# Kernel optimization log

Measured on AMD Instinct MI355X. Metric: run time of the kernel, lower is better.

Reference implementation:

```python
import jax, jax.numpy as jnp
import numpy as np

M1 = 12; M2 = 12; WIDTH = 32; NR = 16; GROUPS = 2; EPS = 1e-5
AND_M = 5; AND_LAM = 1e-4; AND_MAXIT = 16; AND_BETA = 1.0
B = 4; H = 192; W = 192


def group_norm(x, w, b, groups=GROUPS, eps=EPS):
    bb, c, hh, ww = x.shape
    xg = x.reshape(bb, groups, c // groups, hh, ww)
    mu = xg.mean(axis=(2, 3, 4), keepdims=True)
    var = xg.var(axis=(2, 3, 4), keepdims=True)
    xn = ((xg - mu) / jnp.sqrt(var + eps)).reshape(bb, c, hh, ww)
    return xn * w[None, :, None, None] + b[None, :, None, None]


def spectral_conv(z, w1, w2):
    bb, c, hh, ww = z.shape
    zf = jnp.fft.rfft2(z, axes=(-2, -1))  # (B,C,H,W//2+1) complex64
    top = jnp.einsum('bixy,ioxy->boxy', zf[:, :, :M1, :M2], w1)
    bot = jnp.einsum('bixy,ioxy->boxy', zf[:, :, hh - M1:, :M2], w2)
    out = jnp.zeros(zf.shape, zf.dtype)
    out = out.at[:, :, :M1, :M2].set(top).at[:, :, hh - M1:, :M2].set(bot)
    return jnp.fft.irfft2(out, s=(hh, ww), axes=(-2, -1))


def f_block(z, xin, p):
    (conv_w, gnw, gnb, q_w, q_b, w1r, w1i, w2r, w2i,
     w0w, w0b, n1w, n1b, n2w, n2b) = p
    # ConvInjection: conv3x3 -> GroupNorm -> channel Linear -> sigmoid
    xi = jax.lax.conv_general_dilated(xin, conv_w, (1, 1), 'SAME',
                                      dimension_numbers=('NCHW', 'OIHW', 'NCHW'))
    xi = group_norm(xi, gnw, gnb)
    xi = jax.nn.sigmoid(jnp.einsum('bnhw,dn->bdhw', xi, q_w) + q_b[None, :, None, None])
    # FourierLayer: spectral conv + 1x1 conv, gelu
    y1 = spectral_conv(z, jax.lax.complex(w1r, w1i), jax.lax.complex(w2r, w2i))
    y2 = jnp.einsum('bchw,oc->bohw', z, w0w) + w0b[None, :, None, None]
    y = jax.nn.gelu(y1 + y2, approximate=False)
    return group_norm(jax.nn.relu(z + group_norm(xi + y, n1w, n1b)), n2w, n2b)


def anderson(f, x0, m=AND_M, lam=AND_LAM, max_iter=AND_MAXIT, beta=AND_BETA):
    """Anderson acceleration; fixed iteration count (tol early-exit omitted)."""
    shp = x0.shape
    bsz = shp[0]
    fv = lambda v: f(v.reshape(shp)).reshape(bsz, -1)
    x0v = x0.reshape(bsz, -1)
    d = x0v.shape[1]
    f0 = fv(x0v)
    f1 = fv(f0)
    X = jnp.zeros((bsz, m, d), x0.dtype).at[:, 0].set(x0v).at[:, 1].set(f0)
    Fm = jnp.zeros((bsz, m, d), x0.dtype).at[:, 0].set(f0).at[:, 1].set(f1)
    last = 1
    for k in range(2, max_iter):
        n = min(k, m)
        G = Fm[:, :n] - X[:, :n]
        Hk = jnp.zeros((bsz, n + 1, n + 1), x0.dtype)
        Hk = Hk.at[:, 0, 1:].set(1.0).at[:, 1:, 0].set(1.0)
        Hk = Hk.at[:, 1:, 1:].set(jnp.einsum('bnd,bmd->bnm', G, G)
                                  + lam * jnp.eye(n, dtype=x0.dtype)[None])
        yk = jnp.zeros((bsz, n + 1, 1), x0.dtype).at[:, 0, 0].set(1.0)
        alpha = jnp.linalg.solve(Hk, yk)[:, 1:, 0]  # (B, n)
        xnew = (beta * jnp.einsum('bn,bnd->bd', alpha, Fm[:, :n])
                + (1.0 - beta) * jnp.einsum('bn,bnd->bd', alpha, X[:, :n]))
        X = X.at[:, k % m].set(xnew)
        Fm = Fm.at[:, k % m].set(fv(xnew))
        last = k % m
    return X[:, last].reshape(shp)


def setup_inputs():
    key = jax.random.key(0)
    ks = jax.random.split(key, 16)
    scale = 1.0 / (WIDTH * WIDTH)
    u = lambda k, shp, s: jax.random.uniform(k, shp, jnp.float32, -s, s)
    return {
        'x': jax.random.normal(ks[0], (B, 1, H, W), jnp.float32),
        'fc0_w': u(ks[1], (WIDTH, 1), 1.0),
        'fc0_b': u(ks[2], (WIDTH,), 1.0),
        'conv_w': 0.01 * jax.random.normal(ks[3], (NR, WIDTH, 3, 3), jnp.float32),
        'inj_gn_w': jnp.ones((NR,), jnp.float32),
        'inj_gn_b': jnp.zeros((NR,), jnp.float32),
        'q_w': 0.01 * jax.random.normal(ks[4], (WIDTH, NR), jnp.float32),
        'q_b': u(ks[5], (WIDTH,), 0.25),
        'sw1r': scale * jax.random.uniform(ks[6], (WIDTH, WIDTH, M1, M2), jnp.float32),
        'sw1i': scale * jax.random.uniform(ks[7], (WIDTH, WIDTH, M1, M2), jnp.float32),
        'sw2r': scale * jax.random.uniform(ks[8], (WIDTH, WIDTH, M1, M2), jnp.float32),
        'sw2i': scale * jax.random.uniform(ks[9], (WIDTH, WIDTH, M1, M2), jnp.float32),
        'w0_w': u(ks[10], (WIDTH, WIDTH), 1.0 / np.sqrt(WIDTH)),
        'w0_b': u(ks[11], (WIDTH,), 1.0 / np.sqrt(WIDTH)),
        'n1_w': jnp.ones((WIDTH,), jnp.float32),
        'n1_b': jnp.zeros((WIDTH,), jnp.float32),
        'n2_w': jnp.ones((WIDTH,), jnp.float32),
        'n2_b': jnp.zeros((WIDTH,), jnp.float32),
        'bn_w': jnp.ones((WIDTH,), jnp.float32),
        'bn_b': jnp.zeros((WIDTH,), jnp.float32),
        'fc1_w': u(ks[12], (32, WIDTH), 1.0 / np.sqrt(WIDTH)),
        'fc1_b': u(ks[13], (32,), 1.0 / np.sqrt(WIDTH)),
        'fc2_w': u(ks[14], (1, 32), 1.0 / np.sqrt(32.0)),
        'fc2_b': u(ks[15], (1,), 1.0 / np.sqrt(32.0)),
    }


def reference(x, fc0_w, fc0_b, conv_w, inj_gn_w, inj_gn_b, q_w, q_b,
              sw1r, sw1i, sw2r, sw2i, w0_w, w0_b, n1_w, n1_b, n2_w, n2_b,
              bn_w, bn_b, fc1_w, fc1_b, fc2_w, fc2_b):
    xin = jnp.einsum('bchw,oc->bohw', x, fc0_w) + fc0_b[None, :, None, None]
    p = (conv_w, inj_gn_w, inj_gn_b, q_w, q_b, sw1r, sw1i, sw2r, sw2i,
         w0_w, w0_b, n1_w, n1_b, n2_w, n2_b)
    z_star = anderson(lambda z: f_block(z, xin, p), jnp.zeros_like(xin))
    z = f_block(z_star, xin, p)
    # BatchNorm2d (training-mode batch statistics, biased var)
    mu = z.mean(axis=(0, 2, 3), keepdims=True)
    var = z.var(axis=(0, 2, 3), keepdims=True)
    zb = (z - mu) / jnp.sqrt(var + EPS) * bn_w[None, :, None, None] + bn_b[None, :, None, None]
    h1 = jax.nn.gelu(jnp.einsum('bchw,oc->bohw', zb, fc1_w) + fc1_b[None, :, None, None],
                     approximate=False)
    return jnp.einsum('bchw,oc->bohw', h1, fc2_w) + fc2_b[None, :, None, None]
```

## Files before the change

### kernel.cpp

```cpp
#include <hip/hip_runtime.h>
#include <math.h>

#ifndef M_PI
#define M_PI 3.14159265358979323846
#endif

#define BBc 4
#define CCc 32
#define NRk 16
#define HHc 192
#define WWc 192
#define HWc 36864
#define DDi 1179648
#define M1c 12
#define EPSc 1e-5f

static const size_t DDs = (size_t)DDi;

#define SZ_T   ((size_t)4718592)
#define SZ_ZC  ((size_t)589824)
#define SZ_ZF  ((size_t)73728)
#define SZ_WT  ((size_t)589824)
#define SZ_TAB ((size_t)4992)

#define OFF_XC   ((size_t)0)
#define OFF_XI   (OFF_XC + SZ_T)
#define OFF_F    (OFF_XI + SZ_T)
#define OFF_G    (OFF_F + 5 * SZ_T)
#define OFF_ZC   (OFF_G + 5 * SZ_T)
#define OFF_ZF   (OFF_ZC + SZ_ZC)
#define OFF_MO   (OFF_ZF + SZ_ZF)
#define OFF_TM   (OFF_MO + SZ_ZF)
#define OFF_WT   (OFF_TM + SZ_ZC)
#define OFF_TAB  (OFF_WT + SZ_WT)
#define OFF_STAT (OFF_TAB + SZ_TAB)
#define A_XI0  OFF_G

#define NSLICE  32
#define NGSLICE 16
#define ST_EV   1024
#define ST_INJ   (16 * ST_EV)
#define ST_BN    (ST_INJ + 16)
#define ST_GRAM  (ST_BN + 64)
#define ST_ALPHA (ST_GRAM + NGSLICE * 60)
#define ST_TOTAL (ST_ALPHA + 20)

__device__ __forceinline__ float bf2f(unsigned short u) {
    return __uint_as_float(((unsigned int)u) << 16);
}
__device__ __forceinline__ unsigned short f2bf(float f) {
    unsigned int u = __float_as_uint(f);
    unsigned int r = (u + 0x7FFFu + ((u >> 16) & 1u)) >> 16;
    return (unsigned short)r;
}

__global__ void k_zero(float* p, int n) {
    int i = blockIdx.x * blockDim.x + threadIdx.x;
    if (i < n) p[i] = 0.f;
}

__global__ void k_tables(float* tab) {
    int i = blockIdx.x * blockDim.x + threadIdx.x;
    if (i < 13 * 192) {
        int k = i / 192, x = i % 192;
        double th = 2.0 * M_PI * (double)(k * x) / 192.0;
        tab[i] = (float)cos(th);
        tab[13 * 192 + i] = (float)sin(th);
    }
}

__global__ void k_wt(const float* __restrict__ w1r, const float* __restrict__ w1i,
                     const float* __restrict__ w2r, const float* __restrict__ w2i,
                     float* __restrict__ wt) {
    int idx = blockIdx.x * 256 + threadIdx.x;
    if (idx >= 24 * 12 * 1024) return;
    int o = idx & 31;
    int i = (idx >> 5) & 31;
    int ky = (idx >> 10) % 12;
    int j = idx / (12 * 1024);
    const float* wr;
    const float* wi;
    int x;
    if (j < 12) { wr = w1r; wi = w1i; x = j; }
    else        { wr = w2r; wi = w2i; x = j - 12; }
    int src = ((i * 32 + o) * 12 + x) * 12 + ky;
    size_t dst = (((size_t)ky * 24 + j) * 1024 + i * 32 + o) * 2;
    wt[dst] = wr[src];
    wt[dst + 1] = wi[src];
}

__global__ void k_ew(const float* __restrict__ cw, const float* __restrict__ fc0w,
                     const float* __restrict__ fc0b, float* __restrict__ ewb) {
    int i = threadIdx.x;
    if (i >= 144) return;
    int n = i / 9, t = i % 9;
    float ew = 0.f, eb = 0.f;
    for (int c = 0; c < 32; ++c) {
        float k = cw[(size_t)(n * CCc + c) * 9 + t];
        ew += k * fc0w[c];
        eb += k * fc0b[c];
    }
    ewb[i] = ew;
    ewb[144 + i] = eb;
}

__global__ __launch_bounds__(192) void k_conv2(const float* __restrict__ x,
                                               const float* __restrict__ ewb,
                                               float* __restrict__ xi0) {
    int b = blockIdx.x / HHc, h = blockIdx.x % HHc;
    __shared__ float sm[3 * 194];
    __shared__ float ews[144], ebs[144];
    int w = threadIdx.x;
    for (int i = threadIdx.x; i < 3 * 194; i += 192) {
        int r = i / 194, col = (i % 194) - 1;
        int hr = h + r - 1;
        float v = 0.f;
        if (hr >= 0 && hr < HHc && col >= 0 && col < WWc)
            v = x[(size_t)b * HWc + (size_t)hr * WWc + col];
        sm[i] = v;
    }
    if (threadIdx.x < 144) {
        ews[threadIdx.x] = ewb[threadIdx.x];
        ebs[threadIdx.x] = ewb[144 + threadIdx.x];
    }
    __syncthreads();
    float xv[9], mk[9];
#pragma unroll
    for (int r = 0; r < 3; ++r) {
        int hr = h + r - 1;
        bool rok = (hr >= 0 && hr < HHc);
#pragma unroll
        for (int dx = 0; dx < 3; ++dx) {
            int wx = w + dx - 1;
            bool ok = rok && (wx >= 0) && (wx < WWc);
            xv[r * 3 + dx] = sm[r * 194 + (w + dx)];
            mk[r * 3 + dx] = ok ? 1.f : 0.f;
        }
    }
#pragma unroll
    for (int n = 0; n < 16; ++n) {
        float acc = 0.f;
#pragma unroll
        for (int t = 0; t < 9; ++t)
            acc += ews[n * 9 + t] * xv[t] + mk[t] * ebs[n * 9 + t];
        xi0[((size_t)b * NRk + n) * HWc + (size_t)h * WWc + w] = acc;
    }
}

__global__ void k_binstats(const float* __restrict__ src, float* __restrict__ stats,
                           int binsize, int blocksPerBin) {
    int bin = blockIdx.x / blocksPerBin, sub = blockIdx.x % blocksPerBin;
    const float* p = src + (size_t)bin * binsize;
    float s = 0.f, q = 0.f;
    for (int i = sub * blockDim.x + threadIdx.x; i < binsize; i += blocksPerBin * blockDim.x) {
        float v = p[i];
        s += v;
        q += v * v;
    }
    for (int o = 32; o; o >>= 1) { s += __shfl_down(s, o); q += __shfl_down(q, o); }
    __shared__ float rs[4], rq[4];
    int wid = threadIdx.x >> 6, lane = threadIdx.x & 63;
    if (lane == 0) { rs[wid] = s; rq[wid] = q; }
    __syncthreads();
    if (threadIdx.x == 0) {
        int nw = blockDim.x >> 6;
        float ts = 0.f, tq = 0.f;
        for (int i = 0; i < nw; ++i) { ts += rs[i]; tq += rq[i]; }
        atomicAdd(&stats[bin * 2], ts);
        atomicAdd(&stats[bin * 2 + 1], tq);
    }
}

__global__ __launch_bounds__(192) void k_xi(const float* __restrict__ xi0,
                                            const float* __restrict__ stats,
                                            const float* __restrict__ gnw, const float* __restrict__ gnb,
                                            const float* __restrict__ qw, const float* __restrict__ qb,
                                            float* __restrict__ xi) {
    int b = blockIdx.x / HHc, h = blockIdx.x % HHc;
    int w = threadIdx.x;
    const float Ninv = 1.f / (8.f * HWc);
    float tn[16];
#pragma unroll
    for (int n = 0; n < 16; ++n) {
        int g = n >> 3;
        float su = stats[(b * 2 + g) * 2], sq = stats[(b * 2 + g) * 2 + 1];
        float mu = su * Ninv;
        float var = sq * Ninv - mu * mu;
        float inv = rsqrtf(var + EPSc);
        float v = xi0[((size_t)b * NRk + n) * HWc + (size_t)h * WWc + w];
        tn[n] = (v - mu) * inv * gnw[n] + gnb[n];
    }
#pragma unroll
    for (int d = 0; d < 32; ++d) {
        float acc = qb[d];
        const float* row = qw + d * 16;
#pragma unroll
        for (int n = 0; n < 16; ++n) acc += tn[n] * row[n];
        xi[((size_t)b * CCc + d) * HWc + (size_t)h * WWc + w] = 1.f / (1.f + expf(-acc));
    }
}


__global__ __launch_bounds__(192) void k_dftw(const float* __restrict__ z0,
                                              const float* __restrict__ tab,
                                              float* __restrict__ Zc) {
    int bc = blockIdx.x / 24;
    int hg = blockIdx.x % 24;
    int b = bc >> 5, c = bc & 31;
    const float* zp = z0 + (size_t)b * DDs + (size_t)c * HWc + (size_t)hg * 8 * WWc;
    __shared__ float rows[8 * 196];
    __shared__ float tb[24 * 196];
    const float4* zq = (const float4*)zp;
    for (int i4 = threadIdx.x; i4 < 384; i4 += 192) {
        float4 v = zq[i4];
        int r = i4 / 48, col = (i4 % 48) * 4;
        *(float4*)&rows[r * 196 + col] = v;
    }
    for (int i4 = threadIdx.x; i4 < 1152; i4 += 192) {
        int rr = i4 / 48, col = (i4 % 48) * 4;
        const float* src = (rr < 12) ? &tab[rr * 192 + col] : &tab[2496 + (rr - 12) * 192 + col];
        *(float4*)&tb[rr * 196 + col] = *(const float4*)src;
    }
    __syncthreads();
    int t = threadIdx.x;
    int r = t / 24, q = t % 24, ky = q >> 1, isim = q & 1;
    const float* tbp = tb + (isim ? (12 + ky) * 196 : ky * 196);
    const float* rowp = rows + r * 196;
    float a0 = 0.f, a1 = 0.f, a2 = 0.f, a3 = 0.f;
#pragma unroll
    for (int w2 = 0; w2 < WWc; w2 += 4) {
        a0 += rowp[w2] * tbp[w2];
        a1 += rowp[w2 + 1] * tbp[w2 + 1];
        a2 += rowp[w2 + 2] * tbp[w2 + 2];
        a3 += rowp[w2 + 3] * tbp[w2 + 3];
    }
    float acc = (a0 + a1) + (a2 + a3);
    if (isim) acc = -acc;
    int h = hg * 8 + r;
    Zc[(((size_t)ky * 128 + bc) * HHc + h) * 2 + isim] = acc;
}

__global__ __launch_bounds__(192) void k_dftwx(const float* __restrict__ F,
                                               const float* __restrict__ gram,
                                               const float* __restrict__ tab,
                                               float* __restrict__ xc,
                                               float* __restrict__ Zc,
                                               int n) {
    int bc = blockIdx.x / 24;
    int hg = blockIdx.x % 24;
    int b = bc >> 5, c = bc & 31;
    __shared__ float rows[8 * 196];
    __shared__ float tb[24 * 196];
    __shared__ float gs[15];
    __shared__ float alf[5];
    for (int i4 = threadIdx.x; i4 < 1152; i4 += 192) {
        int rr = i4 / 48, col = (i4 % 48) * 4;
        const float* src = (rr < 12) ? &tab[rr * 192 + col] : &tab[2496 + (rr - 12) * 192 + col];
        *(float4*)&tb[rr * 196 + col] = *(const float4*)src;
    }
    if (threadIdx.x < 15) {
        float v = 0.f;
        for (int s2 = 0; s2 < NGSLICE; ++s2) v += gram[s2 * 60 + b * 15 + threadIdx.x];
        gs[threadIdx.x] = v;
    }
    __syncthreads();
    if (threadIdx.x == 0) {
        float H[5][5];
#pragma unroll
        for (int i = 0; i < 5; ++i)
#pragma unroll
            for (int j = 0; j <= i; ++j) {
                float v;
                if (i < n && j < n) v = gs[i * (i + 1) / 2 + j] + ((i == j) ? 1e-4f : 0.f);
                else                v = (i == j) ? 1.f : 0.f;
                H[i][j] = v;
                H[j][i] = v;
            }
        float L[5][5], D[5], w[5], y[5];
#pragma unroll
        for (int j = 0; j < 5; ++j) {
            float d = H[j][j];
#pragma unroll
            for (int k2 = 0; k2 < j; ++k2) d -= L[j][k2] * L[j][k2] * D[k2];
            D[j] = d;
#pragma unroll
            for (int i = j + 1; i < 5; ++i) {
                float v = H[i][j];
#pragma unroll
                for (int k2 = 0; k2 < j; ++k2) v -= L[i][k2] * L[j][k2] * D[k2];
                L[i][j] = v / d;
            }
        }
#pragma unroll
        for (int i = 0; i < 5; ++i) {
            float v = (i < n) ? 1.f : 0.f;
#pragma unroll
            for (int k2 = 0; k2 < i; ++k2) v -= L[i][k2] * w[k2];
            w[i] = v;
        }
#pragma unroll
        for (int i = 4; i >= 0; --i) {
            float v = w[i] / D[i];
#pragma unroll
            for (int k2 = i + 1; k2 < 5; ++k2) v -= L[k2][i] * y[k2];
            y[i] = v;
        }
        float sum = y[0] + y[1] + y[2] + y[3] + y[4];
        float inv = 1.f / sum;
#pragma unroll
        for (int j = 0; j < 5; ++j) alf[j] = (j < n) ? y[j] * inv : 0.f;
    }
    __syncthreads();
    float a0 = alf[0], a1 = alf[1], a2 = alf[2], a3 = alf[3], a4 = alf[4];

    size_t elem = (size_t)b * DDs + (size_t)c * HWc + (size_t)hg * 8 * WWc;
    int off4 = (int)(elem >> 2);
    const int sq4 = 1179648;
    const float4* F4 = (const float4*)F;
    float4* xc4 = (float4*)xc;
    if (n == 5) {
        for (int i4 = threadIdx.x; i4 < 384; i4 += 192) {
            float4 f0 = F4[off4 + i4];
            float4 f1 = F4[sq4 + off4 + i4];
            float4 f2 = F4[2 * sq4 + off4 + i4];
            float4 f3 = F4[3 * sq4 + off4 + i4];
            float4 f4v = F4[4 * sq4 + off4 + i4];
            float4 v;
            v.x = a0 * f0.x + a1 * f1.x + a2 * f2.x + a3 * f3.x + a4 * f4v.x;
            v.y = a0 * f0.y + a1 * f1.y + a2 * f2.y + a3 * f3.y + a4 * f4v.y;
            v.z = a0 * f0.z + a1 * f1.z + a2 * f2.z + a3 * f3.z + a4 * f4v.z;
            v.w = a0 * f0.w + a1 * f1.w + a2 * f2.w + a3 * f3.w + a4 * f4v.w;
            xc4[off4 + i4] = v;
            int r = i4 / 48, col = (i4 % 48) * 4;
            *(float4*)&rows[r * 196 + col] = v;
        }
    } else {
        for (int i4 = threadIdx.x; i4 < 384; i4 += 192) {
            float4 f0 = F4[off4 + i4];
            float4 f1 = F4[sq4 + off4 + i4];
            float4 v;
            v.x = a0 * f0.x + a1 * f1.x;
            v.y = a0 * f0.y + a1 * f1.y;
            v.z = a0 * f0.z + a1 * f1.z;
            v.w = a0 * f0.w + a1 * f1.w;
            if (n >= 3) {
                float4 f2 = F4[2 * sq4 + off4 + i4];
                v.x += a2 * f2.x; v.y += a2 * f2.y; v.z += a2 * f2.z; v.w += a2 * f2.w;
            }
            if (n >= 4) {
                float4 f3 = F4[3 * sq4 + off4 + i4];
                v.x += a3 * f3.x; v.y += a3 * f3.y; v.z += a3 * f3.z; v.w += a3 * f3.w;
            }
            xc4[off4 + i4] = v;
            int r = i4 / 48, col = (i4 % 48) * 4;
            *(float4*)&rows[r * 196 + col] = v;
        }
    }
    __syncthreads();
    int t = threadIdx.x;
    int r = t / 24, q = t % 24, ky = q >> 1, isim = q & 1;
    const float* tbp = tb + (isim ? (12 + ky) * 196 : ky * 196);
    const float* rowp = rows + r * 196;
    float a0s = 0.f, a1s = 0.f, a2s = 0.f, a3s = 0.f;
#pragma unroll
    for (int w2 = 0; w2 < WWc; w2 += 4) {
        a0s += rowp[w2] * tbp[w2];
        a1s += rowp[w2 + 1] * tbp[w2 + 1];
        a2s += rowp[w2 + 2] * tbp[w2 + 2];
        a3s += rowp[w2 + 3] * tbp[w2 + 3];
    }
    float acc = (a0s + a1s) + (a2s + a3s);
    if (isim) acc = -acc;
    int h = hg * 8 + r;
    Zc[(((size_t)ky * 128 + bc) * HHc + h) * 2 + isim] = acc;
}

__global__ __launch_bounds__(192) void k_specA(const float* __restrict__ ZC,
                                               const float* __restrict__ tab,
                                               float* __restrict__ ZF) {
    int kyh = blockIdx.x & 1;
    int c = (blockIdx.x >> 1) & 31;
    int b = blockIdx.x >> 6;
    int bc = b * 32 + c;
    int ky0 = kyh * 6;
    __shared__ float zc[6 * 388];
    __shared__ float tcs[13 * 196];
    __shared__ float tsn[13 * 196];
    int t = threadIdx.x;
    for (int i4 = t; i4 < 576; i4 += 192) {
        int kyl = i4 / 96, r4 = (i4 % 96) * 4;
        *(float4*)&zc[kyl * 388 + r4] =
            *(const float4*)(ZC + (size_t)((ky0 + kyl) * 128 + bc) * 384 + r4);
    }
    for (int i4 = t; i4 < 1248; i4 += 192) {
        int half = i4 / 624, k = (i4 % 624) / 48, col = (i4 % 48) * 4;
        const float* src = tab + half * 2496 + k * 192 + col;
        float* dst = (half ? tsn : tcs) + k * 196 + col;
        *(float4*)dst = *(const float4*)src;
    }
    __syncthreads();
    if (t < 144) {
        int kyl = t / 24, j = t % 24;
        int k = (j < 12) ? j : 24 - j;
        float sgn = (j < 12) ? 1.f : -1.f;
        const float* zp = zc + kyl * 388;
        const float* cp = tcs + k * 196;
        const float* sp = tsn + k * 196;
        float re0 = 0.f, im0 = 0.f, re1 = 0.f, im1 = 0.f;
        for (int h = 0; h < 192; h += 2) {
            float zr = zp[h * 2], zi = zp[h * 2 + 1];
            float cv = cp[h], sv = sgn * sp[h];
            re0 += zr * cv + zi * sv;
            im0 += zi * cv - zr * sv;
            float zr1 = zp[h * 2 + 2], zi1 = zp[h * 2 + 3];
            float cv1 = cp[h + 1], sv1 = sgn * sp[h + 1];
            re1 += zr1 * cv1 + zi1 * sv1;
            im1 += zi1 * cv1 - zr1 * sv1;
        }
        size_t o = (((size_t)(b * 12 + ky0 + kyl) * 24 + j) * 32 + c) * 2;
        ZF[o] = re0 + re1;
        ZF[o + 1] = im0 + im1;
    }
}

__global__ __launch_bounds__(256) void k_specB(const float* __restrict__ ZF,
                                               const float* __restrict__ wt,
                                               const float* __restrict__ tab,
                                               float* __restrict__ Tm) {
    int hq = blockIdx.x & 3;
    int ky = (blockIdx.x >> 2) % 12;
    int b = blockIdx.x / 48;
    __shared__ float zf[24 * 64];
    __shared__ float mo[32 * 50];
    __shared__ float tcs[13 * 48];
    __shared__ float tsn[13 * 48];
    int t = threadIdx.x;
    const float4* zsrc = (const float4*)(ZF + (size_t)(b * 12 + ky) * 1536);
    for (int i4 = t; i4 < 384; i4 += 256)
        *(float4*)&zf[i4 * 4] = zsrc[i4];
    for (int i4 = t; i4 < 312; i4 += 256) {
        int half = i4 / 156, idx = i4 % 156;
        int k = idx / 12, col = (idx % 12) * 4;
        const float* src = tab + half * 2496 + k * 192 + hq * 48 + col;
        float* dst = (half ? tsn : tcs) + k * 48 + col;
        *(float4*)dst = *(const float4*)src;
    }
    __syncthreads();
    const float* wky = wt + (size_t)ky * 24 * 2048;
    for (int p = t; p < 768; p += 256) {
        int j = p / 32, o = p % 32;
        const float* wp = wky + (size_t)j * 2048 + o * 2;
        const float* zj = zf + j * 64;
        float re = 0.f, im = 0.f;
#pragma unroll 8
        for (int i = 0; i < 32; ++i) {
            float ar = zj[i * 2], ai = zj[i * 2 + 1];
            float wr = wp[i * 64], wi = wp[i * 64 + 1];
            re += ar * wr - ai * wi;
            im += ar * wi + ai * wr;
        }
        mo[o * 50 + j * 2] = re;
        mo[o * 50 + j * 2 + 1] = im;
    }
    __syncthreads();
    const float scale = 1.f / 192.f;
    for (int p = t; p < 1536; p += 256) {
        int o = p / 48, hl = p % 48;
        int h = hq * 48 + hl;
        const float* mp = mo + o * 50;
        float re = 0.f, im = 0.f;
#pragma unroll
        for (int j = 0; j < 24; ++j) {
            int k = (j < 12) ? j : 24 - j;
            float sgn = (j < 12) ? 1.f : -1.f;
            float mr = mp[j * 2], mi = mp[j * 2 + 1];
            float cv = tcs[k * 48 + hl], sv = sgn * tsn[k * 48 + hl];
            re += mr * cv - mi * sv;
            im += mr * sv + mi * cv;
        }
        float* dst = Tm + ((size_t)(b * 32 + o) * HHc + h) * 24 + ky * 2;
        dst[0] = re * scale;
        dst[1] = im * scale;
    }
}

__global__ __launch_bounds__(384) void k_f5(const float* __restrict__ z0,
                                            const float* __restrict__ Tm,
                                            const float* __restrict__ xi,
                                            const float* __restrict__ w0w,
                                            const float* __restrict__ w0b,
                                            const float* __restrict__ tab,
                                            float* __restrict__ sbuf,
                                            float* __restrict__ stats_e,
                                            int use_y1) {
    int h = blockIdx.x % HHc;
    int b = blockIdx.x / HHc;
    __shared__ float zl[32 * 192];
    __shared__ float w0s[32 * 36];
    __shared__ float tms[32 * 28];
    __shared__ float redc[6][2];
    int tid = threadIdx.x;
    int oq = tid & 3;
    int wq = (tid >> 2) % 48;
    int oh = tid / 192;
    int w4 = wq * 4;
    int ob = oh * 16 + oq;

    if (z0) {
        const float* zp = z0 + (size_t)b * DDs + (size_t)h * WWc;
        for (int i4 = tid; i4 < 32 * 48; i4 += 384) {
            int c = i4 / 48, q = (i4 % 48) * 4;
            float4 v = *(const float4*)(zp + (size_t)c * HWc + q);
            *(float4*)&zl[c * 192 + q] = v;
        }
        if (tid < 256) {
            int oo = tid >> 3, q = (tid & 7) * 4;
            *(float4*)&w0s[oo * 36 + q] = *(const float4*)(w0w + oo * 32 + q);
        }
    }
    if (use_y1) {
        if (tid < 192) {
            int oo = tid / 6, q = (tid % 6) * 4;
            *(float4*)&tms[oo * 28 + q] =
                *(const float4*)(Tm + (((size_t)b * 32 + oo) * HHc + h) * 24 + q);
        }
    }
    float4 c1r = *(const float4*)(tab + 192 + w4);
    float4 s1r = *(const float4*)(tab + 2496 + 192 + w4);
    __syncthreads();

    const float Winv = 1.f / 192.f;
    float acc[4][4];
#pragma unroll
    for (int oo = 0; oo < 4; ++oo) {
        float bbv = w0b[ob + oo * 4];
#pragma unroll
        for (int k = 0; k < 4; ++k) acc[oo][k] = bbv;
    }
    if (use_y1) {
#pragma unroll
        for (int oo = 0; oo < 4; ++oo) {
            float t0 = tms[(ob + oo * 4) * 28];
#pragma unroll
            for (int k = 0; k < 4; ++k) acc[oo][k] += t0 * Winv;
        }
        float4 ck = c1r, sk = s1r;
        const float sc = 2.f * Winv;
#pragma unroll
        for (int ky = 1; ky <= 11; ++ky) {
#pragma unroll
            for (int oo = 0; oo < 4; ++oo) {
                int o = ob + oo * 4;
                float tre = tms[o * 28 + 2 * ky] * sc;
                float tim = tms[o * 28 + 2 * ky + 1] * sc;
                acc[oo][0] += tre * ck.x - tim * sk.x;
                acc[oo][1] += tre * ck.y - tim * sk.y;
                acc[oo][2] += tre * ck.z - tim * sk.z;
                acc[oo][3] += tre * ck.w - tim * sk.w;
            }
            if (ky < 11) {
                float4 cn, sn;
                cn.x = ck.x * c1r.x - sk.x * s1r.x;
                sn.x = sk.x * c1r.x + ck.x * s1r.x;
                cn.y = ck.y * c1r.y - sk.y * s1r.y;
                sn.y = sk.y * c1r.y + ck.y * s1r.y;
                cn.z = ck.z * c1r.z - sk.z * s1r.z;
                sn.z = sk.z * c1r.z + ck.z * s1r.z;
                cn.w = ck.w * c1r.w - sk.w * s1r.w;
                sn.w = sk.w * c1r.w + ck.w * s1r.w;
                ck = cn; sk = sn;
            }
        }
    }
    if (z0) {
#pragma unroll 2
        for (int c = 0; c < 32; c += 4) {
            float4 wv[4];
#pragma unroll
            for (int oo = 0; oo < 4; ++oo)
                wv[oo] = *(const float4*)&w0s[(ob + oo * 4) * 36 + c];
#pragma unroll
            for (int k = 0; k < 4; ++k) {
                float4 z4 = *(const float4*)&zl[(c + k) * 192 + w4];
#pragma unroll
                for (int oo = 0; oo < 4; ++oo) {
                    float wvk = ((const float*)&wv[oo])[k];
                    acc[oo][0] += z4.x * wvk;
                    acc[oo][1] += z4.y * wvk;
                    acc[oo][2] += z4.z * wvk;
                    acc[oo][3] += z4.w * wvk;
                }
            }
        }
    }
    float4 xv[4];
#pragma unroll
    for (int oo = 0; oo < 4; ++oo) {
        int o = ob + oo * 4;
        xv[oo] = *(const float4*)(xi + (size_t)b * DDs + (size_t)o * HWc +
                                  (size_t)h * WWc + w4);
    }
    float s = 0.f, q = 0.f;
#pragma unroll
    for (int oo = 0; oo < 4; ++oo) {
        int o = ob + oo * 4;
        size_t gi = (size_t)b * DDs + (size_t)o * HWc + (size_t)h * WWc + w4;
        float4 out4;
        float* op = (float*)&out4;
        const float* xp = (const float*)&xv[oo];
#pragma unroll
        for (int k = 0; k < 4; ++k) {
            float v = acc[oo][k];
            float u = 0.5f * v * (1.f + erff(v * 0.70710678118654752f));
            float sv = xp[k] + u;
            op[k] = sv;
            s += sv;
            q += sv * sv;
        }
        *(float4*)(sbuf + gi) = out4;
    }
    for (int o2 = 32; o2; o2 >>= 1) {
        s += __shfl_down(s, o2);
        q += __shfl_down(q, o2);
    }
    int wid = tid >> 6, lane = tid & 63;
    if (lane == 0) { redc[wid][0] = s; redc[wid][1] = q; }
    __syncthreads();
    if (tid == 0) {
        float s0 = redc[0][0] + redc[1][0] + redc[2][0];
        float q0 = redc[0][1] + redc[1][1] + redc[2][1];
        float s1 = redc[3][0] + redc[4][0] + redc[5][0];
        float q1 = redc[3][1] + redc[4][1] + redc[5][1];
        int slice = blockIdx.x & (NSLICE - 1);
        float* st = stats_e + slice * 32;
        atomicAdd(&st[b * 4 + 0], s0);
        atomicAdd(&st[b * 4 + 1], q0);
        atomicAdd(&st[b * 4 + 2], s1);
        atomicAdd(&st[b * 4 + 3], q1);
    }
}

__global__ __launch_bounds__(256) void k_f6(const float* __restrict__ z0,
                                            float* buf,
                                            float* __restrict__ stats_e,
                                            const float* __restrict__ n1w,
                                            const float* __restrict__ n1b,
                                            float* __restrict__ gram,
                                            int slot) {
    {
        int gid = blockIdx.x * 256 + threadIdx.x;
        if (gid < NGSLICE * 20) {
            int s2 = gid / 20, r = gid % 20;
            int j = r % 5, b2 = r / 5;
            int ii = slot > j ? slot : j, jj = slot > j ? j : slot;
            gram[s2 * 60 + b2 * 15 + ii * (ii + 1) / 2 + jj] = 0.f;
        }
    }
    const int binq = 147456;
    const int BPB = 144;
    int bin = blockIdx.x / BPB, sub = blockIdx.x % BPB;
    float Nv = 16.f * HWc;
    float su = 0.f, sq = 0.f;
    for (int s2 = 0; s2 < NSLICE; ++s2) {
        su += stats_e[s2 * 32 + bin * 2];
        sq += stats_e[s2 * 32 + bin * 2 + 1];
    }
    float mu = su / Nv;
    float var = sq / Nv - mu * mu;
    float inv = rsqrtf(var + EPSc);
    const float4* z4 = (const float4*)z0;
    float4* b4 = (float4*)buf;
    float s = 0.f, q = 0.f;
    for (int i4 = sub * 256 + threadIdx.x; i4 < binq; i4 += BPB * 256) {
        int e4 = bin * binq + i4;
        int c = (bin & 1) * 16 + i4 / 9216;
        float w1 = inv * n1w[c];
        float b1 = n1b[c] - mu * w1;
        float4 sv = b4[e4];
        float4 zv = make_float4(0.f, 0.f, 0.f, 0.f);
        if (z0) zv = z4[e4];
        float4 r;
        r.x = zv.x + sv.x * w1 + b1; r.x = r.x > 0.f ? r.x : 0.f;
        r.y = zv.y + sv.y * w1 + b1; r.y = r.y > 0.f ? r.y : 0.f;
        r.z = zv.z + sv.z * w1 + b1; r.z = r.z > 0.f ? r.z : 0.f;
        r.w = zv.w + sv.w * w1 + b1; r.w = r.w > 0.f ? r.w : 0.f;
        b4[e4] = r;
        s += r.x + r.y + r.z + r.w;
        q += r.x * r.x + r.y * r.y + r.z * r.z + r.w * r.w;
    }
    for (int o = 32; o; o >>= 1) { s += __shfl_down(s, o); q += __shfl_down(q, o); }
    __shared__ float rs[4], rq[4];
    int wid = threadIdx.x >> 6, lane = threadIdx.x & 63;
    if (lane == 0) { rs[wid] = s; rq[wid] = q; }
    __syncthreads();
    if (threadIdx.x == 0) {
        int slice = blockIdx.x & (NSLICE - 1);
        atomicAdd(&stats_e[slice * 32 + 16 + bin * 2], rs[0] + rs[1] + rs[2] + rs[3]);
        atomicAdd(&stats_e[slice * 32 + 16 + bin * 2 + 1], rq[0] + rq[1] + rq[2] + rq[3]);
    }
}

__global__ __launch_bounds__(256) void k_f7g(float* buf,
                                             const float* __restrict__ z,
                                             const float* __restrict__ stats_e,
                                             const float* __restrict__ n2w,
                                             const float* __restrict__ n2b,
                                             unsigned short* __restrict__ G,
                                             float* __restrict__ gram,
                                             int slot, int do_gram) {
    int b = blockIdx.x / 288, sub = blockIdx.x % 288;
    const float Ninv = 1.f / (16.f * HWc);
    float su0 = 0.f, sq0 = 0.f, su1 = 0.f, sq1 = 0.f;
    for (int s2 = 0; s2 < NSLICE; ++s2) {
        const float* st = stats_e + s2 * 32 + 16 + b * 4;
        su0 += st[0]; sq0 += st[1]; su1 += st[2]; sq1 += st[3];
    }
    float mu0 = su0 * Ninv, inv0 = rsqrtf(sq0 * Ninv - mu0 * mu0 + EPSc);
    float mu1 = su1 * Ninv, inv1 = rsqrtf(sq1 * Ninv - mu1 * mu1 + EPSc);
    const int bq = 294912;
    const int sq4 = 1179648;
    float4* b4 = (float4*)buf;
    const float4* z4 = (const float4*)z;
    ushort4* GU = (ushort4*)G;
    float p0 = 0, p1 = 0, p2 = 0, p3 = 0, p4 = 0;
    for (int loc4 = sub * 256 + threadIdx.x; loc4 < bq; loc4 += 73728) {
        int e4 = b * bq + loc4;
        int c = loc4 / 9216;
        float mu = (c < 16) ? mu0 : mu1;
        float inv = (c < 16) ? inv0 : inv1;
        float wv = inv * n2w[c];
        float bv = n2b[c] - mu * wv;
        float4 r = b4[e4];
        float4 fn;
        fn.x = r.x * wv + bv;
        fn.y = r.y * wv + bv;
        fn.z = r.z * wv + bv;
        fn.w = r.w * wv + bv;
        b4[e4] = fn;
        if (do_gram) {
            float4 zv = make_float4(0.f, 0.f, 0.f, 0.f);
            if (z) zv = z4[e4];
            float4 g;
            g.x = fn.x - zv.x; g.y = fn.y - zv.y; g.z = fn.z - zv.z; g.w = fn.w - zv.w;
            ushort4 gw;
            gw.x = f2bf(g.x); gw.y = f2bf(g.y); gw.z = f2bf(g.z); gw.w = f2bf(g.w);
            GU[(size_t)slot * sq4 + e4] = gw;
            float4 gj[5];
#pragma unroll
            for (int j = 0; j < 5; ++j) {
                if (j == slot) { gj[j] = g; }
                else {
                    ushort4 u = GU[(size_t)j * sq4 + e4];
                    gj[j].x = bf2f(u.x); gj[j].y = bf2f(u.y);
                    gj[j].z = bf2f(u.z); gj[j].w = bf2f(u.w);
                }
            }
            p0 += g.x * gj[0].x + g.y * gj[0].y + g.z * gj[0].z + g.w * gj[0].w;
            p1 += g.x * gj[1].x + g.y * gj[1].y + g.z * gj[1].z + g.w * gj[1].w;
            p2 += g.x * gj[2].x + g.y * gj[2].y + g.z * gj[2].z + g.w * gj[2].w;
            p3 += g.x * gj[3].x + g.y * gj[3].y + g.z * gj[3].z + g.w * gj[3].w;
            p4 += g.x * gj[4].x + g.y * gj[4].y + g.z * gj[4].z + g.w * gj[4].w;
        }
    }
    if (!do_gram) return;
    float p[5] = {p0, p1, p2, p3, p4};
    __shared__ float red[4][5];
    int wid = threadIdx.x >> 6, lane = threadIdx.x & 63;
#pragma unroll
    for (int j = 0; j < 5; ++j) {
        float v = p[j];
        for (int o = 32; o; o >>= 1) v += __shfl_down(v, o);
        if (lane == 0) red[wid][j] = v;
    }
    __syncthreads();
    if (threadIdx.x == 0) {
        int gsl = (blockIdx.x & (NGSLICE - 1)) * 60;
#pragma unroll
        for (int j = 0; j < 5; ++j) {
            int ii = slot > j ? slot : j, jj = slot > j ? j : slot;
            atomicAdd(&gram[gsl + b * 15 + ii * (ii + 1) / 2 + jj],
                      red[0][j] + red[1][j] + red[2][j] + red[3][j]);
        }
    }
}

__global__ __launch_bounds__(256) void k_bnstats(const float* __restrict__ z,
                                                 float* __restrict__ bstats) {
    const int BPB = 18;
    int c = blockIdx.x / BPB, sub = blockIdx.x % BPB;
    float s = 0.f, q = 0.f;
    for (int i = sub * 256 + threadIdx.x; i < BBc * HWc; i += BPB * 256) {
        int b = i / HWc, hw = i % HWc;
        float v = z[(size_t)b * DDs + (size_t)c * HWc + hw];
        s += v;
        q += v * v;
    }
    for (int o = 32; o; o >>= 1) { s += __shfl_down(s, o); q += __shfl_down(q, o); }
    __shared__ float rs[4], rq[4];
    int wid = threadIdx.x >> 6, lane = threadIdx.x & 63;
    if (lane == 0) { rs[wid] = s; rq[wid] = q; }
    __syncthreads();
    if (threadIdx.x == 0) {
        atomicAdd(&bstats[c * 2], rs[0] + rs[1] + rs[2] + rs[3]);
        atomicAdd(&bstats[c * 2 + 1], rq[0] + rq[1] + rq[2] + rq[3]);
    }
}

__global__ __launch_bounds__(192) void k_final(const float* __restrict__ z,
                                               const float* __restrict__ bstats,
                                               const float* __restrict__ bnw,
                                               const float* __restrict__ bnb,
                                               const float* __restrict__ fc1w,
                                               const float* __restrict__ fc1b,
                                               const float* __restrict__ fc2w,
                                               const float* __restrict__ fc2b,
                                               float* __restrict__ out) {
    int b = blockIdx.x / HHc, h = blockIdx.x % HHc;
    int w = threadIdx.x;
    const float Ninv = 1.f / ((float)BBc * HWc);
    float zv[32];
#pragma unroll
    for (int c = 0; c < 32; ++c) {
        float su = bstats[c * 2], sq = bstats[c * 2 + 1];
        float mu = su * Ninv;
        float var = sq * Ninv - mu * mu;
        float inv = rsqrtf(var + EPSc);
        float v = z[(size_t)b * DDs + (size_t)c * HWc + (size_t)h * WWc + w];
        zv[c] = (v - mu) * inv * bnw[c] + bnb[c];
    }
    float acc2 = fc2b[0];
#pragma unroll
    for (int o = 0; o < 32; ++o) {
        float a = fc1b[o];
        const float* row = fc1w + o * 32;
#pragma unroll
        for (int c = 0; c < 32; ++c) a += zv[c] * row[c];
        float g = 0.5f * a * (1.f + erff(a * 0.70710678118654752f));
        acc2 += fc2w[o] * g;
    }
    out[(size_t)b * HWc + (size_t)h * WWc + w] = acc2;
}

extern "C" void kernel_launch(void* const* d_in, const int* in_sizes, int n_in,
                              void* d_out, int out_size, void* d_ws, size_t ws_size,
                              hipStream_t stream) {
    (void)in_sizes; (void)n_in; (void)out_size; (void)ws_size;
    const float* x    = (const float*)d_in[0];
    const float* fc0w = (const float*)d_in[1];
    const float* fc0b = (const float*)d_in[2];
    const float* convw = (const float*)d_in[3];
    const float* gnw  = (const float*)d_in[4];
    const float* gnb  = (const float*)d_in[5];
    const float* qw   = (const float*)d_in[6];
    const float* qb   = (const float*)d_in[7];
    const float* sw1r = (const float*)d_in[8];
    const float* sw1i = (const float*)d_in[9];
    const float* sw2r = (const float*)d_in[10];
    const float* sw2i = (const float*)d_in[11];
    const float* w0w  = (const float*)d_in[12];
    const float* w0b  = (const float*)d_in[13];
    const float* n1w  = (const float*)d_in[14];
    const float* n1b  = (const float*)d_in[15];
    const float* n2w  = (const float*)d_in[16];
    const float* n2b  = (const float*)d_in[17];
    const float* bnw  = (const float*)d_in[18];
    const float* bnb  = (const float*)d_in[19];
    const float* fc1w = (const float*)d_in[20];
    const float* fc1b = (const float*)d_in[21];
    const float* fc2w = (const float*)d_in[22];
    const float* fc2b = (const float*)d_in[23];
    float* out = (float*)d_out;

    float* ws = (float*)d_ws;
    float* XC  = ws + OFF_XC;
    float* XIp = ws + OFF_XI;
    float* Fb  = ws + OFF_F;
    unsigned short* Gb16 = (unsigned short*)(ws + OFF_G);
    float* ZC  = ws + OFF_ZC;
    float* ZFp = ws + OFF_ZF;
    float* MOp = ws + OFF_MO;
    float* TM  = ws + OFF_TM;
    float* WT  = ws + OFF_WT;
    float* TAB = ws + OFF_TAB;
    float* ST  = ws + OFF_STAT;
    float* XI0 = ws + A_XI0;
    float* EWB = MOp;

    auto runtail = [&](const float* zin, int outslot, int use_y1, int evalIdx,
                       int do_gram) {
        float* dst = Fb + (size_t)outslot * SZ_T;
        if (use_y1) {
            k_specA<<<256, 192, 0, stream>>>(ZC, TAB, ZFp);
            k_specB<<<BBc * 12 * 4, 256, 0, stream>>>(ZFp, WT, TAB, TM);
        }
        float* stats_e = ST + (size_t)evalIdx * ST_EV;
        k_f5<<<BBc * HHc, 384, 0, stream>>>(zin, TM, XIp, w0w, w0b, TAB, dst,
                                            stats_e, use_y1);
        k_f6<<<8 * 144, 256, 0, stream>>>(zin, dst, stats_e, n1w, n1b,
                                          ST + ST_GRAM, outslot);
        k_f7g<<<4 * 288, 256, 0, stream>>>(dst, zin, stats_e, n2w, n2b, Gb16,
                                           ST + ST_GRAM, outslot, do_gram);
    };

    k_tables<<<10, 256, 0, stream>>>(TAB);
    k_wt<<<(24 * 12 * 1024 + 255) / 256, 256, 0, stream>>>(sw1r, sw1i, sw2r, sw2i, WT);
    k_zero<<<(ST_TOTAL + 255) / 256, 256, 0, stream>>>(ST, ST_TOTAL);
    k_ew<<<1, 192, 0, stream>>>(convw, fc0w, fc0b, EWB);
    k_conv2<<<BBc * HHc, 192, 0, stream>>>(x, EWB, XI0);
    k_binstats<<<8 * 36, 256, 0, stream>>>(XI0, ST + ST_INJ, 8 * HWc, 36);
    k_xi<<<BBc * HHc, 192, 0, stream>>>(XI0, ST + ST_INJ, gnw, gnb, qw, qb, XIp);

    runtail(nullptr, 0, 0, 0, 1);
    k_dftw<<<BBc * CCc * 24, 192, 0, stream>>>(Fb, TAB, ZC);
    runtail(Fb, 1, 1, 1, 1);

    for (int k = 2; k < 16; ++k) {
        int n = k < 5 ? k : 5;
        int slot = k % 5;
        k_dftwx<<<BBc * CCc * 24, 192, 0, stream>>>(Fb, ST + ST_GRAM, TAB, XC, ZC, n);
        runtail(XC, slot, 1, k, (k < 15) ? 1 : 0);
    }

    k_bnstats<<<32 * 18, 256, 0, stream>>>(Fb, ST + ST_BN);
    k_final<<<BBc * HHc, 192, 0, stream>>>(Fb, ST + ST_BN, bnw, bnb, fc1w, fc1b,
                                           fc2w, fc2b, out);
}
```

Measured before the change: 1.764 ms.

## Recompute first norm in final pass and skip unused Gram history slots

k_f6 no longer writes the relu(z + GN1) result back to memory and now only accumulates statistics for the second group norm. k_f7g reloads the pre-norm buffer and z and recomputes that value before applying GN2, which removes one full-tensor write and read per evaluation. Gram accumulation now takes a count of valid history slots, so bf16 history reads and atomics for slots that are not yet filled are skipped. The cost is redundant arithmetic, plus a z read in k_f7g even when the Gram is disabled.

```diff
diff --git a/kernel.cpp b/kernel.cpp
--- a/kernel.cpp
+++ b/kernel.cpp
@@ -641,7 +641,7 @@
 }
 
 __global__ __launch_bounds__(256) void k_f6(const float* __restrict__ z0,
-                                            float* buf,
+                                            const float* __restrict__ buf,
                                             float* __restrict__ stats_e,
                                             const float* __restrict__ n1w,
                                             const float* __restrict__ n1b,
@@ -669,7 +669,7 @@
     float var = sq / Nv - mu * mu;
     float inv = rsqrtf(var + EPSc);
     const float4* z4 = (const float4*)z0;
-    float4* b4 = (float4*)buf;
+    const float4* b4 = (const float4*)buf;
     float s = 0.f, q = 0.f;
     for (int i4 = sub * 256 + threadIdx.x; i4 < binq; i4 += BPB * 256) {
         int e4 = bin * binq + i4;
@@ -684,7 +684,6 @@
         r.y = zv.y + sv.y * w1 + b1; r.y = r.y > 0.f ? r.y : 0.f;
         r.z = zv.z + sv.z * w1 + b1; r.z = r.z > 0.f ? r.z : 0.f;
         r.w = zv.w + sv.w * w1 + b1; r.w = r.w > 0.f ? r.w : 0.f;
-        b4[e4] = r;
         s += r.x + r.y + r.z + r.w;
         q += r.x * r.x + r.y * r.y + r.z * r.z + r.w * r.w;
     }
@@ -703,18 +702,25 @@
 __global__ __launch_bounds__(256) void k_f7g(float* buf,
                                              const float* __restrict__ z,
                                              const float* __restrict__ stats_e,
+                                             const float* __restrict__ n1w,
+                                             const float* __restrict__ n1b,
                                              const float* __restrict__ n2w,
                                              const float* __restrict__ n2b,
                                              unsigned short* __restrict__ G,
                                              float* __restrict__ gram,
-                                             int slot, int do_gram) {
+                                             int slot, int nvalid) {
     int b = blockIdx.x / 288, sub = blockIdx.x % 288;
     const float Ninv = 1.f / (16.f * HWc);
+    float s10 = 0.f, q10 = 0.f, s11 = 0.f, q11 = 0.f;
     float su0 = 0.f, sq0 = 0.f, su1 = 0.f, sq1 = 0.f;
     for (int s2 = 0; s2 < NSLICE; ++s2) {
-        const float* st = stats_e + s2 * 32 + 16 + b * 4;
-        su0 += st[0]; sq0 += st[1]; su1 += st[2]; sq1 += st[3];
-    }
+        const float* st1 = stats_e + s2 * 32 + b * 4;
+        s10 += st1[0]; q10 += st1[1]; s11 += st1[2]; q11 += st1[3];
+        const float* st2 = stats_e + s2 * 32 + 16 + b * 4;
+        su0 += st2[0]; sq0 += st2[1]; su1 += st2[2]; sq1 += st2[3];
+    }
+    float mu10 = s10 * Ninv, i10 = rsqrtf(q10 * Ninv - mu10 * mu10 + EPSc);
+    float mu11 = s11 * Ninv, i11 = rsqrtf(q11 * Ninv - mu11 * mu11 + EPSc);
     float mu0 = su0 * Ninv, inv0 = rsqrtf(sq0 * Ninv - mu0 * mu0 + EPSc);
     float mu1 = su1 * Ninv, inv1 = rsqrtf(sq1 * Ninv - mu1 * mu1 + EPSc);
     const int bq = 294912;
@@ -726,20 +732,28 @@
     for (int loc4 = sub * 256 + threadIdx.x; loc4 < bq; loc4 += 73728) {
         int e4 = b * bq + loc4;
         int c = loc4 / 9216;
-        float mu = (c < 16) ? mu0 : mu1;
-        float inv = (c < 16) ? inv0 : inv1;
+        float mu1g, i1g, mu, inv;
+        if (c < 16) { mu1g = mu10; i1g = i10; mu = mu0; inv = inv0; }
+        else        { mu1g = mu11; i1g = i11; mu = mu1; inv = inv1; }
+        float w1 = i1g * n1w[c];
+        float b1 = n1b[c] - mu1g * w1;
         float wv = inv * n2w[c];
         float bv = n2b[c] - mu * wv;
-        float4 r = b4[e4];
+        float4 sv = b4[e4];
+        float4 zv = make_float4(0.f, 0.f, 0.f, 0.f);
+        if (z) zv = z4[e4];
+        float4 r;
+        r.x = zv.x + sv.x * w1 + b1; r.x = r.x > 0.f ? r.x : 0.f;
+        r.y = zv.y + sv.y * w1 + b1; r.y = r.y > 0.f ? r.y : 0.f;
+        r.z = zv.z + sv.z * w1 + b1; r.z = r.z > 0.f ? r.z : 0.f;
+        r.w = zv.w + sv.w * w1 + b1; r.w = r.w > 0.f ? r.w : 0.f;
         float4 fn;
         fn.x = r.x * wv + bv;
         fn.y = r.y * wv + bv;
         fn.z = r.z * wv + bv;
         fn.w = r.w * wv + bv;
         b4[e4] = fn;
-        if (do_gram) {
-            float4 zv = make_float4(0.f, 0.f, 0.f, 0.f);
-            if (z) zv = z4[e4];
+        if (nvalid) {
             float4 g;
             g.x = fn.x - zv.x; g.y = fn.y - zv.y; g.z = fn.z - zv.z; g.w = fn.w - zv.w;
             ushort4 gw;
@@ -748,7 +762,8 @@
             float4 gj[5];
 #pragma unroll
             for (int j = 0; j < 5; ++j) {
-                if (j == slot) { gj[j] = g; }
+                if (j >= nvalid) { gj[j] = make_float4(0.f, 0.f, 0.f, 0.f); }
+                else if (j == slot) { gj[j] = g; }
                 else {
                     ushort4 u = GU[(size_t)j * sq4 + e4];
                     gj[j].x = bf2f(u.x); gj[j].y = bf2f(u.y);
@@ -762,7 +777,7 @@
             p4 += g.x * gj[4].x + g.y * gj[4].y + g.z * gj[4].z + g.w * gj[4].w;
         }
     }
-    if (!do_gram) return;
+    if (!nvalid) return;
     float p[5] = {p0, p1, p2, p3, p4};
     __shared__ float red[4][5];
     int wid = threadIdx.x >> 6, lane = threadIdx.x & 63;
@@ -777,6 +792,7 @@
         int gsl = (blockIdx.x & (NGSLICE - 1)) * 60;
 #pragma unroll
         for (int j = 0; j < 5; ++j) {
+            if (j >= nvalid) continue;
             int ii = slot > j ? slot : j, jj = slot > j ? j : slot;
             atomicAdd(&gram[gsl + b * 15 + ii * (ii + 1) / 2 + jj],
                       red[0][j] + red[1][j] + red[2][j] + red[3][j]);
@@ -887,7 +903,7 @@
     float* EWB = MOp;
 
     auto runtail = [&](const float* zin, int outslot, int use_y1, int evalIdx,
-                       int do_gram) {
+                       int nvalid) {
         float* dst = Fb + (size_t)outslot * SZ_T;
         if (use_y1) {
             k_specA<<<256, 192, 0, stream>>>(ZC, TAB, ZFp);
@@ -898,8 +914,8 @@
                                             stats_e, use_y1);
         k_f6<<<8 * 144, 256, 0, stream>>>(zin, dst, stats_e, n1w, n1b,
                                           ST + ST_GRAM, outslot);
-        k_f7g<<<4 * 288, 256, 0, stream>>>(dst, zin, stats_e, n2w, n2b, Gb16,
-                                           ST + ST_GRAM, outslot, do_gram);
+        k_f7g<<<4 * 288, 256, 0, stream>>>(dst, zin, stats_e, n1w, n1b, n2w, n2b,
+                                           Gb16, ST + ST_GRAM, outslot, nvalid);
     };
 
     k_tables<<<10, 256, 0, stream>>>(TAB);
@@ -912,13 +928,14 @@
 
     runtail(nullptr, 0, 0, 0, 1);
     k_dftw<<<BBc * CCc * 24, 192, 0, stream>>>(Fb, TAB, ZC);
-    runtail(Fb, 1, 1, 1, 1);
+    runtail(Fb, 1, 1, 1, 2);
 
     for (int k = 2; k < 16; ++k) {
         int n = k < 5 ? k : 5;
         int slot = k % 5;
+        int nv = (k < 15) ? ((k + 1 < 5) ? (k + 1) : 5) : 0;
         k_dftwx<<<BBc * CCc * 24, 192, 0, stream>>>(Fb, ST + ST_GRAM, TAB, XC, ZC, n);
-        runtail(XC, slot, 1, k, (k < 15) ? 1 : 0);
+        runtail(XC, slot, 1, k, nv);
     }
 
     k_bnstats<<<32 * 18, 256, 0, stream>>>(Fb, ST + ST_BN);
```

Result: no change. 1.782 ms (+1.0%).
